# Performance work log

Measured on AMD Instinct MI355X. Metric: run time of the kernel, lower is better.

Reference implementation:

```python
import jax, jax.numpy as jnp
import numpy as np

N, E, CIN, COUT = 100000, 1600000, 64, 128
EPS = 1e-5  # torch BatchNorm default


def setup_inputs() -> dict:
    key = jax.random.key(0)
    ks = jax.random.split(key, 16)
    s = 0.1
    x = jax.random.normal(ks[0], (N, CIN), jnp.float32)
    src = jax.random.randint(ks[1], (E,), 0, N, dtype=jnp.int32)
    dst = jax.random.randint(ks[2], (E,), 0, N, dtype=jnp.int32)
    edge_index = jnp.stack([src, dst])  # [2, E]
    return {
        "x": x,
        "edge_index": edge_index,
        # conv0: GraphConv(CIN -> COUT)
        "W_root0": jax.random.normal(ks[3], (COUT, CIN), jnp.float32) * s,
        "W_nbr0": jax.random.normal(ks[4], (COUT, CIN), jnp.float32) * s,
        "b0": jnp.zeros((COUT,), jnp.float32),
        # bn0
        "g0": jnp.ones((COUT,), jnp.float32),
        "be0": jnp.zeros((COUT,), jnp.float32),
        # conv1: GraphConv(COUT -> COUT)
        "W_root1": jax.random.normal(ks[5], (COUT, COUT), jnp.float32) * s,
        "W_nbr1": jax.random.normal(ks[6], (COUT, COUT), jnp.float32) * s,
        "b1": jnp.zeros((COUT,), jnp.float32),
        # bn1
        "g1": jnp.ones((COUT,), jnp.float32),
        "be1": jnp.zeros((COUT,), jnp.float32),
        # residual 1x1 conv (Conv1d(CIN, COUT, 1))
        "Wlin": jax.random.normal(ks[7], (COUT, CIN), jnp.float32) * s,
        "blin": jnp.zeros((COUT,), jnp.float32),
    }


def graph_conv(x, src, dst, W_root, W_nbr, b):
    # PyG GraphConv: out_i = W_root x_i + W_nbr * sum_{j: (j->i) in E} x_j + b
    agg = jax.ops.segment_sum(x[src], dst, num_segments=N)  # scatter-add over edges
    return x @ W_root.T + agg @ W_nbr.T + b


def batch_norm(x, gamma, beta):
    # training-mode BatchNorm over the node dimension (biased variance)
    mu = jnp.mean(x, axis=0)
    var = jnp.mean(jnp.square(x - mu), axis=0)
    return (x - mu) * jax.lax.rsqrt(var + EPS) * gamma + beta


def reference(x, edge_index, W_root0, W_nbr0, b0, g0, be0,
              W_root1, W_nbr1, b1, g1, be1, Wlin, blin):
    src, dst = edge_index[0], edge_index[1]
    y = batch_norm(graph_conv(x, src, dst, W_root0, W_nbr0, b0), g0, be0)
    y = jax.nn.relu(y)
    y = batch_norm(graph_conv(y, src, dst, W_root1, W_nbr1, b1), g1, be1)
    out = y + (x @ Wlin.T + blin)  # 1x1 Conv1d residual projection
    return jax.nn.relu(out)
```

## Files before the change

kernel.cpp:

```cpp
#include <hip/hip_runtime.h>
#include <stdint.h>


#define CIN 64
#define COUT 128
#define BN_EPS 1e-5f
#define CURPAD 32
#define PCPAD 32
#define SPAD 32
#define PSH 8
#define PNODES (1 << PSH)
#define MAXP 512

typedef unsigned short u16;
typedef short short8 __attribute__((ext_vector_type(8)));
typedef float f32x4 __attribute__((ext_vector_type(4)));

__device__ __forceinline__ float bf2f(u16 u) {
    union { unsigned int i; float f; } v; v.i = ((unsigned int)u) << 16; return v.f;
}
__device__ __forceinline__ u16 f2bf(float f) {
    union { float f; unsigned int i; } v; v.f = f;
    unsigned int r = v.i + 0x7fffu + ((v.i >> 16) & 1u);
    return (u16)(r >> 16);
}
__device__ __forceinline__ float lo16(unsigned int w) { return bf2f((u16)(w & 0xffffu)); }
__device__ __forceinline__ float hi16(unsigned int w) { return bf2f((u16)(w >> 16)); }

template<bool BF> __device__ __forceinline__ float ldf(const void* p, long i) {
    if (BF) return bf2f(((const u16*)p)[i]);
    return ((const float*)p)[i];
}
template<bool BF> __device__ __forceinline__ short8 ld8(const void* p, long i) {
    if (BF) return *(const short8*)((const u16*)p + i);
    const float* f = (const float*)p + i;
    short8 r;
#pragma unroll
    for (int j = 0; j < 8; ++j) r[j] = (short)f2bf(f[j]);
    return r;
}

__device__ __forceinline__ void acc8(float* a, uint4 w) {
    a[0] += lo16(w.x); a[1] += hi16(w.x);
    a[2] += lo16(w.y); a[3] += hi16(w.y);
    a[4] += lo16(w.z); a[5] += hi16(w.z);
    a[6] += lo16(w.w); a[7] += hi16(w.w);
}

__global__ void k_detect(const unsigned int* __restrict__ x, int* __restrict__ flag) {
    int lane = threadIdx.x;
    int cnt = 0;
#pragma unroll
    for (int i = 0; i < 8; ++i) {
        unsigned int w = x[lane * 8 + i];
        unsigned int e0 = (w >> 7) & 0xFFu, e1 = (w >> 23) & 0xFFu;
        cnt += (e0 >= 0x60u && e0 <= 0x8Eu);
        cnt += (e1 >= 0x60u && e1 <= 0x8Eu);
    }
    for (int o = 32; o; o >>= 1) cnt += __shfl_down(cnt, o);
    if (lane == 0) *flag = (cnt > 850) ? 1 : 0;
}

__global__ __launch_bounds__(256) void k_phist(const int* __restrict__ dst,
                                               int* __restrict__ pcount, int E, int np) {
    __shared__ int h[MAXP];
    for (int i = threadIdx.x; i < np; i += 256) h[i] = 0;
    __syncthreads();
    int stride = gridDim.x * 256;
    for (int e = blockIdx.x * 256 + threadIdx.x; e < E; e += stride)
        atomicAdd(&h[dst[e] >> PSH], 1);
    __syncthreads();
    for (int i = threadIdx.x; i < np; i += 256)
        if (h[i]) atomicAdd(&pcount[i * PCPAD], h[i]);
}

__global__ void k_pscan(const int* __restrict__ pcount, int* __restrict__ pstart,
                        int* __restrict__ pcursor, int np, int E) {
    __shared__ int s[MAXP];
    int t = threadIdx.x;
    int v = (t < np) ? pcount[t * PCPAD] : 0;
    s[t] = v; __syncthreads();
    for (int o = 1; o < MAXP; o <<= 1) {
        int u = (t >= o) ? s[t - o] : 0;
        __syncthreads(); s[t] += u; __syncthreads();
    }
    if (t < np) {
        int ex = s[t] - v;
        pstart[t] = ex;
        pcursor[t * CURPAD] = ex;
    }
    if (t == 0) pstart[np] = E;
}

__global__ __launch_bounds__(256) void k_pfill(const int* __restrict__ src,
        const int* __restrict__ dst, int* __restrict__ pcursor,
        unsigned int* __restrict__ barr, int E, int np) {
    __shared__ int cnt[MAXP], gb[MAXP], loc[MAXP];
    int tid = threadIdx.x;
    int base = blockIdx.x * 4096;
    for (int i = tid; i < np; i += 256) { cnt[i] = 0; loc[i] = 0; }
    __syncthreads();
    int pk[16]; unsigned int rec[16];
#pragma unroll
    for (int k = 0; k < 16; ++k) {
        int e = base + k * 256 + tid;
        if (e < E) {
            int d = dst[e];
            pk[k] = d >> PSH;
            rec[k] = ((unsigned int)(d & (PNODES - 1)) << 20) | (unsigned int)src[e];
            atomicAdd(&cnt[pk[k]], 1);
        } else pk[k] = -1;
    }
    __syncthreads();
    for (int i = tid; i < np; i += 256)
        if (cnt[i]) gb[i] = atomicAdd(&pcursor[i * CURPAD], cnt[i]);
    __syncthreads();
#pragma unroll
    for (int k = 0; k < 16; ++k) {
        if (pk[k] >= 0) {
            int off = atomicAdd(&loc[pk[k]], 1);
            barr[gb[pk[k]] + off] = rec[k];
        }
    }
}

__global__ __launch_bounds__(256) void k_psort(const unsigned int* __restrict__ barr,
        const int* __restrict__ pstart, int* __restrict__ csr,
        int* __restrict__ row_start, int n, int np, int E) {
    __shared__ int hist[PNODES], curs[PNODES], tsum[256];
    int tid = threadIdx.x;
    int p = blockIdx.x;
    int e0 = pstart[p], e1 = pstart[p + 1];
    int node0 = p << PSH;
    hist[tid] = 0;
    __syncthreads();
    for (int t = e0 + tid; t < e1; t += 256)
        atomicAdd(&hist[barr[t] >> 20], 1);
    __syncthreads();
    int v = hist[tid];
    tsum[tid] = v; __syncthreads();
    for (int o = 1; o < 256; o <<= 1) {
        int u = (tid >= o) ? tsum[tid - o] : 0;
        __syncthreads(); tsum[tid] += u; __syncthreads();
    }
    int ex = tsum[tid] - v;
    curs[tid] = ex;
    int nd = node0 + tid;
    if (nd < n) row_start[nd] = e0 + ex;
    if (p == np - 1 && tid == 0) row_start[n] = E;
    __syncthreads();
    for (int t = e0 + tid; t < e1; t += 256) {
        unsigned int rec = barr[t];
        int pos = atomicAdd(&curs[rec >> 20], 1);
        csr[e0 + pos] = (int)(rec & 0xFFFFF);
    }
}

template<bool BF>
__device__ __forceinline__ void agg0_impl(const void* x, const int* rs, const int* csr,
                                          u16* agg, int n) {
    int i = blockIdx.x * 4 + (threadIdx.x >> 6);
    if (i >= n) return;
    int lane = threadIdx.x & 63;
    int slot = lane >> 4, cp = lane & 15;
    int b = rs[i], e = rs[i + 1];
    if (BF) {
        const unsigned int* x32 = (const unsigned int*)x;
        float acc[4] = {0.f, 0.f, 0.f, 0.f};
        int t = b + slot;
        for (; t + 12 < e; t += 16) {
            int j0 = csr[t], j1 = csr[t + 4], j2 = csr[t + 8], j3 = csr[t + 12];
            uint2 w0 = *((const uint2*)(x32 + (long)j0 * 32) + cp);
            uint2 w1 = *((const uint2*)(x32 + (long)j1 * 32) + cp);
            uint2 w2 = *((const uint2*)(x32 + (long)j2 * 32) + cp);
            uint2 w3 = *((const uint2*)(x32 + (long)j3 * 32) + cp);
            acc[0] += lo16(w0.x) + lo16(w1.x); acc[1] += hi16(w0.x) + hi16(w1.x);
            acc[2] += lo16(w0.y) + lo16(w1.y); acc[3] += hi16(w0.y) + hi16(w1.y);
            acc[0] += lo16(w2.x) + lo16(w3.x); acc[1] += hi16(w2.x) + hi16(w3.x);
            acc[2] += lo16(w2.y) + lo16(w3.y); acc[3] += hi16(w2.y) + hi16(w3.y);
        }
        for (; t < e; t += 4) {
            int j0 = csr[t];
            uint2 w0 = *((const uint2*)(x32 + (long)j0 * 32) + cp);
            acc[0] += lo16(w0.x); acc[1] += hi16(w0.x);
            acc[2] += lo16(w0.y); acc[3] += hi16(w0.y);
        }
#pragma unroll
        for (int k = 0; k < 4; ++k) {
            acc[k] += __shfl_xor(acc[k], 16);
            acc[k] += __shfl_xor(acc[k], 32);
        }
        if (slot == 0) {
            uint2 o;
            o.x = (unsigned int)f2bf(acc[0]) | ((unsigned int)f2bf(acc[1]) << 16);
            o.y = (unsigned int)f2bf(acc[2]) | ((unsigned int)f2bf(acc[3]) << 16);
            *((uint2*)((unsigned int*)agg + (long)i * 32) + cp) = o;
        }
    } else {
        float acc[4] = {0.f, 0.f, 0.f, 0.f};
        int t = b + slot;
        for (; t + 12 < e; t += 16) {
            int j0 = csr[t], j1 = csr[t + 4], j2 = csr[t + 8], j3 = csr[t + 12];
            float4 w0 = *((const float4*)((const float*)x + (long)j0 * 64) + cp);
            float4 w1 = *((const float4*)((const float*)x + (long)j1 * 64) + cp);
            float4 w2 = *((const float4*)((const float*)x + (long)j2 * 64) + cp);
            float4 w3 = *((const float4*)((const float*)x + (long)j3 * 64) + cp);
            acc[0] += (w0.x + w1.x) + (w2.x + w3.x);
            acc[1] += (w0.y + w1.y) + (w2.y + w3.y);
            acc[2] += (w0.z + w1.z) + (w2.z + w3.z);
            acc[3] += (w0.w + w1.w) + (w2.w + w3.w);
        }
        for (; t < e; t += 4) {
            int j0 = csr[t];
            float4 w0 = *((const float4*)((const float*)x + (long)j0 * 64) + cp);
            acc[0] += w0.x; acc[1] += w0.y; acc[2] += w0.z; acc[3] += w0.w;
        }
#pragma unroll
        for (int k = 0; k < 4; ++k) {
            acc[k] += __shfl_xor(acc[k], 16);
            acc[k] += __shfl_xor(acc[k], 32);
        }
        if (slot == 0) {
            uint2 o;
            o.x = (unsigned int)f2bf(acc[0]) | ((unsigned int)f2bf(acc[1]) << 16);
            o.y = (unsigned int)f2bf(acc[2]) | ((unsigned int)f2bf(acc[3]) << 16);
            *((uint2*)((unsigned int*)agg + (long)i * 32) + cp) = o;
        }
    }
}

__global__ __launch_bounds__(256) void k_agg0(const int* __restrict__ flag,
        const void* x, const int* __restrict__ rs, const int* __restrict__ csr,
        u16* __restrict__ agg, int n) {
    if (*flag) agg0_impl<true >(x, rs, csr, agg, n);
    else       agg0_impl<false>(x, rs, csr, agg, n);
}

__global__ __launch_bounds__(256) void k_y0p(unsigned int* __restrict__ y0,
        const float* __restrict__ sc, const float* __restrict__ sh, long nq) {
    long idx = (long)blockIdx.x * 256 + threadIdx.x;
    int colq = threadIdx.x & 15;
    float s8[8], h8[8];
#pragma unroll
    for (int j = 0; j < 8; ++j) { s8[j] = sc[colq * 8 + j]; h8[j] = sh[colq * 8 + j]; }
    long stride = (long)gridDim.x * 256;
    uint4* p = (uint4*)y0;
    for (; idx < nq; idx += stride) {
        uint4 w = p[idx];
        unsigned int r[4] = {w.x, w.y, w.z, w.w};
        uint4 o;
        unsigned int* po = (unsigned int*)&o;
#pragma unroll
        for (int d = 0; d < 4; ++d) {
            float a = fmaxf(lo16(r[d]) * s8[2 * d]     + h8[2 * d],     0.f);
            float b = fmaxf(hi16(r[d]) * s8[2 * d + 1] + h8[2 * d + 1], 0.f);
            po[d] = (unsigned int)f2bf(a) | ((unsigned int)f2bf(b) << 16);
        }
        p[idx] = o;
    }
}

__global__ __launch_bounds__(256) void k_agg1(const u16* __restrict__ y0p,
        const int* __restrict__ rs, const int* __restrict__ csr,
        u16* __restrict__ agg, int n) {
    int i0 = blockIdx.x * 8 + ((threadIdx.x >> 6) << 1);
    if (i0 >= n) return;
    int lane = threadIdx.x & 63;
    int slot = lane >> 4, cp = lane & 15;
    const unsigned int* y32 = (const unsigned int*)y0p;
    int i1 = i0 + 1;
    int bA = rs[i0], eA = rs[i0 + 1];
    int bB = eA, eB = (i1 < n) ? rs[i1 + 1] : eA;

    float aA[8] = {0.f, 0.f, 0.f, 0.f, 0.f, 0.f, 0.f, 0.f};
    float aB[8] = {0.f, 0.f, 0.f, 0.f, 0.f, 0.f, 0.f, 0.f};
    int tA = bA + slot, tB = bB + slot;

    while (tA + 12 < eA && tB + 12 < eB) {
        int ja0 = csr[tA], ja1 = csr[tA + 4], ja2 = csr[tA + 8], ja3 = csr[tA + 12];
        int jb0 = csr[tB], jb1 = csr[tB + 4], jb2 = csr[tB + 8], jb3 = csr[tB + 12];
        uint4 wa0 = *((const uint4*)(y32 + (long)ja0 * 64) + cp);
        uint4 wa1 = *((const uint4*)(y32 + (long)ja1 * 64) + cp);
        uint4 wa2 = *((const uint4*)(y32 + (long)ja2 * 64) + cp);
        uint4 wa3 = *((const uint4*)(y32 + (long)ja3 * 64) + cp);
        uint4 wb0 = *((const uint4*)(y32 + (long)jb0 * 64) + cp);
        uint4 wb1 = *((const uint4*)(y32 + (long)jb1 * 64) + cp);
        uint4 wb2 = *((const uint4*)(y32 + (long)jb2 * 64) + cp);
        uint4 wb3 = *((const uint4*)(y32 + (long)jb3 * 64) + cp);
        acc8(aA, wa0); acc8(aA, wa1); acc8(aA, wa2); acc8(aA, wa3);
        acc8(aB, wb0); acc8(aB, wb1); acc8(aB, wb2); acc8(aB, wb3);
        tA += 16; tB += 16;
    }
    for (; tA + 12 < eA; tA += 16) {
        int j0 = csr[tA], j1 = csr[tA + 4], j2 = csr[tA + 8], j3 = csr[tA + 12];
        uint4 w0 = *((const uint4*)(y32 + (long)j0 * 64) + cp);
        uint4 w1 = *((const uint4*)(y32 + (long)j1 * 64) + cp);
        uint4 w2 = *((const uint4*)(y32 + (long)j2 * 64) + cp);
        uint4 w3 = *((const uint4*)(y32 + (long)j3 * 64) + cp);
        acc8(aA, w0); acc8(aA, w1); acc8(aA, w2); acc8(aA, w3);
    }
    for (; tA < eA; tA += 4) {
        uint4 w0 = *((const uint4*)(y32 + (long)csr[tA] * 64) + cp);
        acc8(aA, w0);
    }
    for (; tB + 12 < eB; tB += 16) {
        int j0 = csr[tB], j1 = csr[tB + 4], j2 = csr[tB + 8], j3 = csr[tB + 12];
        uint4 w0 = *((const uint4*)(y32 + (long)j0 * 64) + cp);
        uint4 w1 = *((const uint4*)(y32 + (long)j1 * 64) + cp);
        uint4 w2 = *((const uint4*)(y32 + (long)j2 * 64) + cp);
        uint4 w3 = *((const uint4*)(y32 + (long)j3 * 64) + cp);
        acc8(aB, w0); acc8(aB, w1); acc8(aB, w2); acc8(aB, w3);
    }
    for (; tB < eB; tB += 4) {
        uint4 w0 = *((const uint4*)(y32 + (long)csr[tB] * 64) + cp);
        acc8(aB, w0);
    }
#pragma unroll
    for (int k = 0; k < 8; ++k) {
        aA[k] += __shfl_xor(aA[k], 16);
        aA[k] += __shfl_xor(aA[k], 32);
        aB[k] += __shfl_xor(aB[k], 16);
        aB[k] += __shfl_xor(aB[k], 32);
    }
    if (slot == 0) {
        uint4 o;
        o.x = (unsigned int)f2bf(aA[0]) | ((unsigned int)f2bf(aA[1]) << 16);
        o.y = (unsigned int)f2bf(aA[2]) | ((unsigned int)f2bf(aA[3]) << 16);
        o.z = (unsigned int)f2bf(aA[4]) | ((unsigned int)f2bf(aA[5]) << 16);
        o.w = (unsigned int)f2bf(aA[6]) | ((unsigned int)f2bf(aA[7]) << 16);
        *((uint4*)((unsigned int*)agg + (long)i0 * 64) + cp) = o;
        if (i1 < n) {
            uint4 p;
            p.x = (unsigned int)f2bf(aB[0]) | ((unsigned int)f2bf(aB[1]) << 16);
            p.y = (unsigned int)f2bf(aB[2]) | ((unsigned int)f2bf(aB[3]) << 16);
            p.z = (unsigned int)f2bf(aB[4]) | ((unsigned int)f2bf(aB[5]) << 16);
            p.w = (unsigned int)f2bf(aB[6]) | ((unsigned int)f2bf(aB[7]) << 16);
            *((uint4*)((unsigned int*)agg + (long)i1 * 64) + cp) = p;
        }
    }
}

template<bool BF>
__device__ __forceinline__ void gemm0_impl(const void* x, const u16* agg,
                                           const void* Wr, const void* Wn,
                                           u16* y0, float* sumP, float* sqP,
                                           int n, int nch, u16* lds) {
    const int ST = 130;
    int tid = threadIdx.x;
    int wave = tid >> 6, lane = tid & 63, lr = lane & 15, q = lane >> 4;

    short8 wf[2][4];
#pragma unroll
    for (int i = 0; i < 2; ++i) {
        int c = (2 * wave + i) * 16 + lr;
#pragma unroll
        for (int ks = 0; ks < 4; ++ks) {
            const void* W = (ks < 2) ? Wr : Wn;
            wf[i][ks] = ld8<BF>(W, (long)c * CIN + (ks & 1) * 32 + q * 8);
        }
    }

    const int rowb = tid >> 3, wb = tid & 7;
    const int rowf = tid >> 4, wfc = tid & 15;
    short8 rbx[2]; float4 rfx[4]; short8 rag[2];

    auto regload = [&](long chunk0) {
        if (BF) {
#pragma unroll
            for (int i = 0; i < 2; ++i) {
                long rg = chunk0 + rowb + i * 32; if (rg > n - 1) rg = n - 1;
                rbx[i] = *(const short8*)((const u16*)x + rg * CIN + wb * 8);
            }
        } else {
#pragma unroll
            for (int i = 0; i < 4; ++i) {
                long rg = chunk0 + rowf + i * 16; if (rg > n - 1) rg = n - 1;
                rfx[i] = *(const float4*)((const float*)x + rg * CIN + wfc * 4);
            }
        }
#pragma unroll
        for (int i = 0; i < 2; ++i) {
            long rg = chunk0 + rowb + i * 32; if (rg > n - 1) rg = n - 1;
            rag[i] = *(const short8*)(agg + rg * CIN + wb * 8);
        }
    };

    float st[2] = {0.f, 0.f}, sq[2] = {0.f, 0.f};
    int ch = blockIdx.x;
    if (ch < nch) regload((long)ch * 64);
    for (; ch < nch; ch += gridDim.x) {
        long chunk0 = (long)ch * 64;
        __syncthreads();
        if (BF) {
#pragma unroll
            for (int i = 0; i < 2; ++i)
                *(short8*)(lds + (rowb + i * 32) * ST + wb * 8) = rbx[i];
        } else {
#pragma unroll
            for (int i = 0; i < 4; ++i) {
                u16* d = lds + (rowf + i * 16) * ST + wfc * 4;
                d[0] = f2bf(rfx[i].x); d[1] = f2bf(rfx[i].y);
                d[2] = f2bf(rfx[i].z); d[3] = f2bf(rfx[i].w);
            }
        }
#pragma unroll
        for (int i = 0; i < 2; ++i)
            *(short8*)(lds + (rowb + i * 32) * ST + 64 + wb * 8) = rag[i];
        __syncthreads();
        long nxt = (long)ch + gridDim.x;
        if (nxt < nch) regload(nxt * 64);

#pragma unroll
        for (int t = 0; t < 4; ++t) {
            short8 a[4];
#pragma unroll
            for (int ks = 0; ks < 4; ++ks)
                a[ks] = *(const short8*)(lds + (t * 16 + lr) * ST + ks * 32 + q * 8);
#pragma unroll
            for (int i = 0; i < 2; ++i) {
                f32x4 acc = {0.f, 0.f, 0.f, 0.f};
#pragma unroll
                for (int ks = 0; ks < 4; ++ks)
                    acc = __builtin_amdgcn_mfma_f32_16x16x32_bf16(a[ks], wf[i][ks], acc, 0, 0, 0);
                int c = (2 * wave + i) * 16 + lr;
#pragma unroll
                for (int r = 0; r < 4; ++r) {
                    long row = chunk0 + t * 16 + q * 4 + r;
                    if (row < n) {
                        y0[row * COUT + c] = f2bf(acc[r]);
                        st[i] += acc[r]; sq[i] += acc[r] * acc[r];
                    }
                }
            }
        }
    }
#pragma unroll
    for (int i = 0; i < 2; ++i) {
        st[i] += __shfl_xor(st[i], 16); st[i] += __shfl_xor(st[i], 32);
        sq[i] += __shfl_xor(sq[i], 16); sq[i] += __shfl_xor(sq[i], 32);
    }
    if (q == 0) {
#pragma unroll
        for (int i = 0; i < 2; ++i) {
            int c = (2 * wave + i) * 16 + lr;
            atomicAdd(&sumP[c * SPAD], st[i]);
            atomicAdd(&sqP[c * SPAD], sq[i]);
        }
    }
}

__global__ __launch_bounds__(256) void k_gemm0(const int* __restrict__ flag,
        const void* x, const u16* __restrict__ agg, const void* Wr, const void* Wn,
        u16* __restrict__ y0, float* __restrict__ sumP, float* __restrict__ sqP,
        int n, int nch) {
    __shared__ u16 lds[64 * 130];
    if (*flag) gemm0_impl<true >(x, agg, Wr, Wn, y0, sumP, sqP, n, nch, lds);
    else       gemm0_impl<false>(x, agg, Wr, Wn, y0, sumP, sqP, n, nch, lds);
}

template<bool BF>
__device__ __forceinline__ void gemm1_impl(const u16* y0p, const u16* agg,
                                           const void* Wr, const void* Wn,
                                           u16* y1, float* sumP, float* sqP,
                                           int n, int nch) {
    int tid = threadIdx.x;
    int wave = tid >> 6, lane = tid & 63, lr = lane & 15, q = lane >> 4;

    short8 wf[2][8];
#pragma unroll
    for (int i = 0; i < 2; ++i) {
        int c = (2 * wave + i) * 16 + lr;
#pragma unroll
        for (int ks = 0; ks < 8; ++ks) {
            const void* W = (ks < 4) ? Wr : Wn;
            wf[i][ks] = ld8<BF>(W, (long)c * COUT + (ks & 3) * 32 + q * 8);
        }
    }

    float st[2] = {0.f, 0.f}, sq[2] = {0.f, 0.f};
    for (int ch = blockIdx.x; ch < nch; ch += gridDim.x) {
        long chunk0 = (long)ch * 64;
#pragma unroll
        for (int t = 0; t < 4; ++t) {
            long rg = chunk0 + t * 16 + lr; if (rg > n - 1) rg = n - 1;
            short8 a[8];
#pragma unroll
            for (int ks = 0; ks < 4; ++ks)
                a[ks] = *(const short8*)(y0p + rg * COUT + ks * 32 + q * 8);
#pragma unroll
            for (int ks = 0; ks < 4; ++ks)
                a[4 + ks] = *(const short8*)(agg + rg * COUT + ks * 32 + q * 8);
#pragma unroll
            for (int i = 0; i < 2; ++i) {
                f32x4 acc = {0.f, 0.f, 0.f, 0.f};
#pragma unroll
                for (int ks = 0; ks < 8; ++ks)
                    acc = __builtin_amdgcn_mfma_f32_16x16x32_bf16(a[ks], wf[i][ks], acc, 0, 0, 0);
                int c = (2 * wave + i) * 16 + lr;
#pragma unroll
                for (int r = 0; r < 4; ++r) {
                    long row = chunk0 + t * 16 + q * 4 + r;
                    if (row < n) {
                        y1[row * COUT + c] = f2bf(acc[r]);
                        st[i] += acc[r]; sq[i] += acc[r] * acc[r];
                    }
                }
            }
        }
    }
#pragma unroll
    for (int i = 0; i < 2; ++i) {
        st[i] += __shfl_xor(st[i], 16); st[i] += __shfl_xor(st[i], 32);
        sq[i] += __shfl_xor(sq[i], 16); sq[i] += __shfl_xor(sq[i], 32);
    }
    if (q == 0) {
#pragma unroll
        for (int i = 0; i < 2; ++i) {
            int c = (2 * wave + i) * 16 + lr;
            atomicAdd(&sumP[c * SPAD], st[i]);
            atomicAdd(&sqP[c * SPAD], sq[i]);
        }
    }
}

__global__ __launch_bounds__(256) void k_gemm1(const int* __restrict__ flag,
        const u16* __restrict__ y0p, const u16* __restrict__ agg,
        const void* Wr, const void* Wn,
        u16* y1_bf , u16* y1_ws,
        float* __restrict__ sumP, float* __restrict__ sqP, int n, int nch) {
    u16* y1 = *flag ? y1_bf : y1_ws;
    if (*flag) gemm1_impl<true >(y0p, agg, Wr, Wn, y1, sumP, sqP, n, nch);
    else       gemm1_impl<false>(y0p, agg, Wr, Wn, y1, sumP, sqP, n, nch);
}

__global__ void k_bnfin(const int* __restrict__ flag,
                        const float* __restrict__ sumP, const float* __restrict__ sqP,
                        const void* g, const void* be,
                        float* __restrict__ scale, float* __restrict__ shift, int n) {
    int c = threadIdx.x;
    bool bf = (*flag != 0);
    float inv = 1.f / (float)n;
    float mu = sumP[c * SPAD] * inv;
    float var = fmaxf(sqP[c * SPAD] * inv - mu * mu, 0.f);
    float gv = bf ? bf2f(((const u16*)g)[c]) : ((const float*)g)[c];
    float bv = bf ? bf2f(((const u16*)be)[c]) : ((const float*)be)[c];
    float sc = gv * rsqrtf(var + BN_EPS);
    scale[c] = sc;
    shift[c] = bv - mu * sc;
}

template<bool BF>
__device__ __forceinline__ void final_impl(const void* x, const u16* y1,
                                           const void* Wlin, const void* blin,
                                           const float* sc, const float* sh,
                                           void* out, int n, int nch, u16* lds) {
    const int ST = 194;
    int tid = threadIdx.x;
    int wave = tid >> 6, lane = tid & 63, lr = lane & 15, q = lane >> 4;

    short8 wf[2][2];
    float blc[2], scc[2], shc[2];
#pragma unroll
    for (int i = 0; i < 2; ++i) {
        int c = (2 * wave + i) * 16 + lr;
#pragma unroll
        for (int ks = 0; ks < 2; ++ks)
            wf[i][ks] = ld8<BF>(Wlin, (long)c * CIN + ks * 32 + q * 8);
        blc[i] = ldf<BF>(blin, c);
        scc[i] = sc[c]; shc[i] = sh[c];
    }

    const int rowb = tid >> 3, wb = tid & 7;
    const int rowf = tid >> 4, wfc = tid & 15;
    const int rowy = tid >> 4, wy = tid & 15;
    short8 rbx[2]; float4 rfx[4]; short8 ry[4];

    auto regload = [&](long chunk0) {
        if (BF) {
#pragma unroll
            for (int i = 0; i < 2; ++i) {
                long rg = chunk0 + rowb + i * 32; if (rg > n - 1) rg = n - 1;
                rbx[i] = *(const short8*)((const u16*)x + rg * CIN + wb * 8);
            }
        } else {
#pragma unroll
            for (int i = 0; i < 4; ++i) {
                long rg = chunk0 + rowf + i * 16; if (rg > n - 1) rg = n - 1;
                rfx[i] = *(const float4*)((const float*)x + rg * CIN + wfc * 4);
            }
        }
#pragma unroll
        for (int i = 0; i < 4; ++i) {
            long rg = chunk0 + rowy + i * 16; if (rg > n - 1) rg = n - 1;
            ry[i] = *(const short8*)(y1 + rg * COUT + wy * 8);
        }
    };

    int ch = blockIdx.x;
    if (ch < nch) regload((long)ch * 64);
    for (; ch < nch; ch += gridDim.x) {
        long chunk0 = (long)ch * 64;
        __syncthreads();
        if (BF) {
#pragma unroll
            for (int i = 0; i < 2; ++i)
                *(short8*)(lds + (rowb + i * 32) * ST + wb * 8) = rbx[i];
        } else {
#pragma unroll
            for (int i = 0; i < 4; ++i) {
                u16* d = lds + (rowf + i * 16) * ST + wfc * 4;
                d[0] = f2bf(rfx[i].x); d[1] = f2bf(rfx[i].y);
                d[2] = f2bf(rfx[i].z); d[3] = f2bf(rfx[i].w);
            }
        }
#pragma unroll
        for (int i = 0; i < 4; ++i)
            *(short8*)(lds + (rowy + i * 16) * ST + 64 + wy * 8) = ry[i];
        __syncthreads();
        long nxt = (long)ch + gridDim.x;
        if (nxt < nch) regload(nxt * 64);

#pragma unroll
        for (int t = 0; t < 4; ++t) {
            short8 a[2];
#pragma unroll
            for (int ks = 0; ks < 2; ++ks)
                a[ks] = *(const short8*)(lds + (t * 16 + lr) * ST + ks * 32 + q * 8);
#pragma unroll
            for (int i = 0; i < 2; ++i) {
                f32x4 acc = {0.f, 0.f, 0.f, 0.f};
                acc = __builtin_amdgcn_mfma_f32_16x16x32_bf16(a[0], wf[i][0], acc, 0, 0, 0);
                acc = __builtin_amdgcn_mfma_f32_16x16x32_bf16(a[1], wf[i][1], acc, 0, 0, 0);
                int c = (2 * wave + i) * 16 + lr;
#pragma unroll
                for (int r = 0; r < 4; ++r) {
                    long row = chunk0 + t * 16 + q * 4 + r;
                    if (row < n) {
                        float yv = bf2f(lds[(t * 16 + q * 4 + r) * ST + 64 + c]);
                        float v = acc[r] + blc[i] + yv * scc[i] + shc[i];
                        v = fmaxf(v, 0.f);
                        if (BF) ((u16*)out)[row * COUT + c] = f2bf(v);
                        else    ((float*)out)[row * COUT + c] = v;
                    }
                }
            }
        }
    }
}

__global__ __launch_bounds__(256) void k_final(const int* __restrict__ flag,
        const void* x, const void* Wlin, const void* blin,
        const u16* y1_bf , const u16* y1_ws,
        const float* __restrict__ sc, const float* __restrict__ sh,
        void* out, int n, int nch) {
    __shared__ u16 lds[64 * 194];
    const u16* y1 = *flag ? y1_bf : y1_ws;
    if (*flag) final_impl<true >(x, y1, Wlin, blin, sc, sh, out, n, nch, lds);
    else       final_impl<false>(x, y1, Wlin, blin, sc, sh, out, n, nch, lds);
}

extern "C" void kernel_launch(void* const* d_in, const int* in_sizes, int n_in,
                              void* d_out, int out_size, void* d_ws, size_t ws_size,
                              hipStream_t stream) {
    (void)n_in; (void)out_size; (void)ws_size;
    const void* x    = d_in[0];
    const int*  ei   = (const int*)d_in[1];
    const void* Wr0  = d_in[2];
    const void* Wn0  = d_in[3];
    const void* g0   = d_in[5];
    const void* be0  = d_in[6];
    const void* Wr1  = d_in[7];
    const void* Wn1  = d_in[8];
    const void* g1   = d_in[10];
    const void* be1  = d_in[11];
    const void* Wlin = d_in[12];
    const void* blin = d_in[13];

    const int N = in_sizes[0] / CIN;
    const int E = in_sizes[1] / 2;
    const int* src = ei;
    const int* dst = ei + E;
    const int NP = (N + PNODES - 1) >> PSH;

    char* base = (char*)d_ws;
    size_t off = 0;
    auto carve = [&](size_t bytes) -> void* {
        void* p = base + off;
        off = (off + bytes + 255) & ~(size_t)255;
        return p;
    };
    int*   flag      = (int*)carve(256);
    int*   pcount    = (int*)carve(MAXP * PCPAD * sizeof(int));
    int*   pstart    = (int*)carve((MAXP + 1) * sizeof(int));
    int*   pcursor   = (int*)carve(MAXP * CURPAD * sizeof(int));
    float* statsP    = (float*)carve(4 * 128 * SPAD * sizeof(float));
    float* scsh      = (float*)carve(512 * sizeof(float));
    int*   row_start = (int*)carve((size_t)(N + 1) * sizeof(int));
    unsigned int* barr = (unsigned int*)carve((size_t)E * sizeof(int));
    int*   csr       = (int*)carve((size_t)E * sizeof(int));
    u16*   aggu      = (u16*)carve((size_t)N * COUT * sizeof(u16));
    u16*   y0        = (u16*)carve((size_t)N * COUT * sizeof(u16));
    u16*   y1_ws     = (u16*)carve((size_t)N * COUT * sizeof(u16));

    float* sum0P = statsP;
    float* sq0P  = statsP + 128 * SPAD;
    float* sum1P = statsP + 256 * SPAD;
    float* sq1P  = statsP + 384 * SPAD;

    hipMemsetAsync(pcount, 0, MAXP * PCPAD * sizeof(int), stream);
    hipMemsetAsync(statsP, 0, 4 * 128 * SPAD * sizeof(float), stream);

    const int nwb = (N + 3) / 4;
    const int nwb2 = (N + 7) / 8;
    const int nch = (N + 63) / 64;
    const int ntl = (E + 4095) / 4096;
    const int G   = nch < 1024 ? nch : 1024;
    const long nq = (long)N * 16;
    int g2 = (int)((nq + 255) / 256); if (g2 > 2048) g2 = 2048;

    k_detect<<<1, 64, 0, stream>>>((const unsigned int*)x, flag);

    k_phist<<<256, 256, 0, stream>>>(dst, pcount, E, NP);
    k_pscan<<<1, MAXP, 0, stream>>>(pcount, pstart, pcursor, NP, E);
    k_pfill<<<ntl, 256, 0, stream>>>(src, dst, pcursor, barr, E, NP);
    k_psort<<<NP, 256, 0, stream>>>(barr, pstart, csr, row_start, N, NP, E);

    k_agg0 <<<nwb, 256, 0, stream>>>(flag, x, row_start, csr, aggu, N);
    k_gemm0<<<G, 256, 0, stream>>>(flag, x, aggu, Wr0, Wn0, y0,
                                   sum0P, sq0P, N, nch);
    k_bnfin<<<1, 128, 0, stream>>>(flag, sum0P, sq0P, g0, be0,
                                   scsh, scsh + 128, N);

    k_y0p<<<g2, 256, 0, stream>>>((unsigned int*)y0, scsh, scsh + 128, nq);

    k_agg1 <<<nwb2, 256, 0, stream>>>(y0, row_start, csr, aggu, N);
    k_gemm1<<<G, 256, 0, stream>>>(flag, y0, aggu, Wr1, Wn1,
                                   (u16*)d_out, y1_ws, sum1P, sq1P, N, nch);
    k_bnfin<<<1, 128, 0, stream>>>(flag, sum1P, sq1P, g1, be1,
                                   scsh + 256, scsh + 384, N);

    k_final<<<G, 256, 0, stream>>>(flag, x, Wlin, blin,
                                   (const u16*)d_out, y1_ws,
                                   scsh + 256, scsh + 384, d_out, N, nch);
}
```

Baseline: 402.6 us.

## Pre-convert x to bf16 once and read it directly in aggregation and GEMMs

Adds a kernel that converts x to a bf16 copy up front, so agg0, gemm0 and final all read a compact bf16 array. This removes the per-kernel fp32/bf16 branches and the LDS staging of x. gemm0 now loads its A fragments straight from global memory with no LDS or register prefetch, and agg1 goes back to one node per wave. The cost is an extra pass over x, and the gemm0 loads may be less coalesced with less latency hiding.

New measurement: 393.1 us. 1.02x faster.

```diff
diff --git a/kernel.cpp b/kernel.cpp
--- a/kernel.cpp
+++ b/kernel.cpp
@@ -61,6 +61,28 @@
     if (lane == 0) *flag = (cnt > 850) ? 1 : 0;
 }
 
+__global__ __launch_bounds__(256) void k_xbf(const int* __restrict__ flag,
+        const void* __restrict__ x, u16* __restrict__ xb, long n8) {
+    long idx = (long)blockIdx.x * 256 + threadIdx.x;
+    long stride = (long)gridDim.x * 256;
+    uint4* dst = (uint4*)xb;
+    if (*flag) {
+        const uint4* src = (const uint4*)x;
+        for (; idx < n8; idx += stride) dst[idx] = src[idx];
+    } else {
+        const float4* src = (const float4*)x;
+        for (; idx < n8; idx += stride) {
+            float4 a = src[idx * 2], b = src[idx * 2 + 1];
+            uint4 o;
+            o.x = (unsigned int)f2bf(a.x) | ((unsigned int)f2bf(a.y) << 16);
+            o.y = (unsigned int)f2bf(a.z) | ((unsigned int)f2bf(a.w) << 16);
+            o.z = (unsigned int)f2bf(b.x) | ((unsigned int)f2bf(b.y) << 16);
+            o.w = (unsigned int)f2bf(b.z) | ((unsigned int)f2bf(b.w) << 16);
+            dst[idx] = o;
+        }
+    }
+}
+
 __global__ __launch_bounds__(256) void k_phist(const int* __restrict__ dst,
                                                int* __restrict__ pcount, int E, int np) {
     __shared__ int h[MAXP];
@@ -156,84 +178,45 @@
     }
 }
 
-template<bool BF>
-__device__ __forceinline__ void agg0_impl(const void* x, const int* rs, const int* csr,
-                                          u16* agg, int n) {
+__global__ __launch_bounds__(256) void k_agg0(const u16* __restrict__ xb,
+        const int* __restrict__ rs, const int* __restrict__ csr,
+        u16* __restrict__ agg, int n) {
     int i = blockIdx.x * 4 + (threadIdx.x >> 6);
     if (i >= n) return;
     int lane = threadIdx.x & 63;
     int slot = lane >> 4, cp = lane & 15;
+    const unsigned int* x32 = (const unsigned int*)xb;
     int b = rs[i], e = rs[i + 1];
-    if (BF) {
-        const unsigned int* x32 = (const unsigned int*)x;
-        float acc[4] = {0.f, 0.f, 0.f, 0.f};
-        int t = b + slot;
-        for (; t + 12 < e; t += 16) {
-            int j0 = csr[t], j1 = csr[t + 4], j2 = csr[t + 8], j3 = csr[t + 12];
-            uint2 w0 = *((const uint2*)(x32 + (long)j0 * 32) + cp);
-            uint2 w1 = *((const uint2*)(x32 + (long)j1 * 32) + cp);
-            uint2 w2 = *((const uint2*)(x32 + (long)j2 * 32) + cp);
-            uint2 w3 = *((const uint2*)(x32 + (long)j3 * 32) + cp);
-            acc[0] += lo16(w0.x) + lo16(w1.x); acc[1] += hi16(w0.x) + hi16(w1.x);
-            acc[2] += lo16(w0.y) + lo16(w1.y); acc[3] += hi16(w0.y) + hi16(w1.y);
-            acc[0] += lo16(w2.x) + lo16(w3.x); acc[1] += hi16(w2.x) + hi16(w3.x);
-            acc[2] += lo16(w2.y) + lo16(w3.y); acc[3] += hi16(w2.y) + hi16(w3.y);
-        }
-        for (; t < e; t += 4) {
-            int j0 = csr[t];
-            uint2 w0 = *((const uint2*)(x32 + (long)j0 * 32) + cp);
-            acc[0] += lo16(w0.x); acc[1] += hi16(w0.x);
-            acc[2] += lo16(w0.y); acc[3] += hi16(w0.y);
-        }
-#pragma unroll
-        for (int k = 0; k < 4; ++k) {
-            acc[k] += __shfl_xor(acc[k], 16);
-            acc[k] += __shfl_xor(acc[k], 32);
-        }
-        if (slot == 0) {
-            uint2 o;
-            o.x = (unsigned int)f2bf(acc[0]) | ((unsigned int)f2bf(acc[1]) << 16);
-            o.y = (unsigned int)f2bf(acc[2]) | ((unsigned int)f2bf(acc[3]) << 16);
-            *((uint2*)((unsigned int*)agg + (long)i * 32) + cp) = o;
-        }
-    } else {
-        float acc[4] = {0.f, 0.f, 0.f, 0.f};
-        int t = b + slot;
-        for (; t + 12 < e; t += 16) {
-            int j0 = csr[t], j1 = csr[t + 4], j2 = csr[t + 8], j3 = csr[t + 12];
-            float4 w0 = *((const float4*)((const float*)x + (long)j0 * 64) + cp);
-            float4 w1 = *((const float4*)((const float*)x + (long)j1 * 64) + cp);
-            float4 w2 = *((const float4*)((const float*)x + (long)j2 * 64) + cp);
-            float4 w3 = *((const float4*)((const float*)x + (long)j3 * 64) + cp);
-            acc[0] += (w0.x + w1.x) + (w2.x + w3.x);
-            acc[1] += (w0.y + w1.y) + (w2.y + w3.y);
-            acc[2] += (w0.z + w1.z) + (w2.z + w3.z);
-            acc[3] += (w0.w + w1.w) + (w2.w + w3.w);
-        }
-        for (; t < e; t += 4) {
-            int j0 = csr[t];
-            float4 w0 = *((const float4*)((const float*)x + (long)j0 * 64) + cp);
-            acc[0] += w0.x; acc[1] += w0.y; acc[2] += w0.z; acc[3] += w0.w;
-        }
-#pragma unroll
-        for (int k = 0; k < 4; ++k) {
-            acc[k] += __shfl_xor(acc[k], 16);
-            acc[k] += __shfl_xor(acc[k], 32);
-        }
-        if (slot == 0) {
-            uint2 o;
-            o.x = (unsigned int)f2bf(acc[0]) | ((unsigned int)f2bf(acc[1]) << 16);
-            o.y = (unsigned int)f2bf(acc[2]) | ((unsigned int)f2bf(acc[3]) << 16);
-            *((uint2*)((unsigned int*)agg + (long)i * 32) + cp) = o;
-        }
-    }
-}
-
-__global__ __launch_bounds__(256) void k_agg0(const int* __restrict__ flag,
-        const void* x, const int* __restrict__ rs, const int* __restrict__ csr,
-        u16* __restrict__ agg, int n) {
-    if (*flag) agg0_impl<true >(x, rs, csr, agg, n);
-    else       agg0_impl<false>(x, rs, csr, agg, n);
+    float acc[4] = {0.f, 0.f, 0.f, 0.f};
+    int t = b + slot;
+    for (; t + 12 < e; t += 16) {
+        int j0 = csr[t], j1 = csr[t + 4], j2 = csr[t + 8], j3 = csr[t + 12];
+        uint2 w0 = *((const uint2*)(x32 + (long)j0 * 32) + cp);
+        uint2 w1 = *((const uint2*)(x32 + (long)j1 * 32) + cp);
+        uint2 w2 = *((const uint2*)(x32 + (long)j2 * 32) + cp);
+        uint2 w3 = *((const uint2*)(x32 + (long)j3 * 32) + cp);
+        acc[0] += lo16(w0.x) + lo16(w1.x); acc[1] += hi16(w0.x) + hi16(w1.x);
+        acc[2] += lo16(w0.y) + lo16(w1.y); acc[3] += hi16(w0.y) + hi16(w1.y);
+        acc[0] += lo16(w2.x) + lo16(w3.x); acc[1] += hi16(w2.x) + hi16(w3.x);
+        acc[2] += lo16(w2.y) + lo16(w3.y); acc[3] += hi16(w2.y) + hi16(w3.y);
+    }
+    for (; t < e; t += 4) {
+        int j0 = csr[t];
+        uint2 w0 = *((const uint2*)(x32 + (long)j0 * 32) + cp);
+        acc[0] += lo16(w0.x); acc[1] += hi16(w0.x);
+        acc[2] += lo16(w0.y); acc[3] += hi16(w0.y);
+    }
+#pragma unroll
+    for (int k = 0; k < 4; ++k) {
+        acc[k] += __shfl_xor(acc[k], 16);
+        acc[k] += __shfl_xor(acc[k], 32);
+    }
+    if (slot == 0) {
+        uint2 o;
+        o.x = (unsigned int)f2bf(acc[0]) | ((unsigned int)f2bf(acc[1]) << 16);
+        o.y = (unsigned int)f2bf(acc[2]) | ((unsigned int)f2bf(acc[3]) << 16);
+        *((uint2*)((unsigned int*)agg + (long)i * 32) + cp) = o;
+    }
 }
 
 __global__ __launch_bounds__(256) void k_y0p(unsigned int* __restrict__ y0,
@@ -263,89 +246,47 @@
 __global__ __launch_bounds__(256) void k_agg1(const u16* __restrict__ y0p,
         const int* __restrict__ rs, const int* __restrict__ csr,
         u16* __restrict__ agg, int n) {
-    int i0 = blockIdx.x * 8 + ((threadIdx.x >> 6) << 1);
-    if (i0 >= n) return;
+    int i = blockIdx.x * 4 + (threadIdx.x >> 6);
+    if (i >= n) return;
     int lane = threadIdx.x & 63;
     int slot = lane >> 4, cp = lane & 15;
     const unsigned int* y32 = (const unsigned int*)y0p;
-    int i1 = i0 + 1;
-    int bA = rs[i0], eA = rs[i0 + 1];
-    int bB = eA, eB = (i1 < n) ? rs[i1 + 1] : eA;
-
-    float aA[8] = {0.f, 0.f, 0.f, 0.f, 0.f, 0.f, 0.f, 0.f};
-    float aB[8] = {0.f, 0.f, 0.f, 0.f, 0.f, 0.f, 0.f, 0.f};
-    int tA = bA + slot, tB = bB + slot;
-
-    while (tA + 12 < eA && tB + 12 < eB) {
-        int ja0 = csr[tA], ja1 = csr[tA + 4], ja2 = csr[tA + 8], ja3 = csr[tA + 12];
-        int jb0 = csr[tB], jb1 = csr[tB + 4], jb2 = csr[tB + 8], jb3 = csr[tB + 12];
-        uint4 wa0 = *((const uint4*)(y32 + (long)ja0 * 64) + cp);
-        uint4 wa1 = *((const uint4*)(y32 + (long)ja1 * 64) + cp);
-        uint4 wa2 = *((const uint4*)(y32 + (long)ja2 * 64) + cp);
-        uint4 wa3 = *((const uint4*)(y32 + (long)ja3 * 64) + cp);
-        uint4 wb0 = *((const uint4*)(y32 + (long)jb0 * 64) + cp);
-        uint4 wb1 = *((const uint4*)(y32 + (long)jb1 * 64) + cp);
-        uint4 wb2 = *((const uint4*)(y32 + (long)jb2 * 64) + cp);
-        uint4 wb3 = *((const uint4*)(y32 + (long)jb3 * 64) + cp);
-        acc8(aA, wa0); acc8(aA, wa1); acc8(aA, wa2); acc8(aA, wa3);
-        acc8(aB, wb0); acc8(aB, wb1); acc8(aB, wb2); acc8(aB, wb3);
-        tA += 16; tB += 16;
-    }
-    for (; tA + 12 < eA; tA += 16) {
-        int j0 = csr[tA], j1 = csr[tA + 4], j2 = csr[tA + 8], j3 = csr[tA + 12];
+    int b = rs[i], e = rs[i + 1];
+    float acc[8] = {0.f, 0.f, 0.f, 0.f, 0.f, 0.f, 0.f, 0.f};
+    int t = b + slot;
+    for (; t + 12 < e; t += 16) {
+        int j0 = csr[t], j1 = csr[t + 4], j2 = csr[t + 8], j3 = csr[t + 12];
         uint4 w0 = *((const uint4*)(y32 + (long)j0 * 64) + cp);
         uint4 w1 = *((const uint4*)(y32 + (long)j1 * 64) + cp);
         uint4 w2 = *((const uint4*)(y32 + (long)j2 * 64) + cp);
         uint4 w3 = *((const uint4*)(y32 + (long)j3 * 64) + cp);
-        acc8(aA, w0); acc8(aA, w1); acc8(aA, w2); acc8(aA, w3);
-    }
-    for (; tA < eA; tA += 4) {
-        uint4 w0 = *((const uint4*)(y32 + (long)csr[tA] * 64) + cp);
-        acc8(aA, w0);
-    }
-    for (; tB + 12 < eB; tB += 16) {
-        int j0 = csr[tB], j1 = csr[tB + 4], j2 = csr[tB + 8], j3 = csr[tB + 12];
+        acc8(acc, w0); acc8(acc, w1); acc8(acc, w2); acc8(acc, w3);
+    }
+    for (; t < e; t += 4) {
+        int j0 = csr[t];
         uint4 w0 = *((const uint4*)(y32 + (long)j0 * 64) + cp);
-        uint4 w1 = *((const uint4*)(y32 + (long)j1 * 64) + cp);
-        uint4 w2 = *((const uint4*)(y32 + (long)j2 * 64) + cp);
-        uint4 w3 = *((const uint4*)(y32 + (long)j3 * 64) + cp);
-        acc8(aB, w0); acc8(aB, w1); acc8(aB, w2); acc8(aB, w3);
-    }
-    for (; tB < eB; tB += 4) {
-        uint4 w0 = *((const uint4*)(y32 + (long)csr[tB] * 64) + cp);
-        acc8(aB, w0);
+        acc8(acc, w0);
     }
 #pragma unroll
     for (int k = 0; k < 8; ++k) {
-        aA[k] += __shfl_xor(aA[k], 16);
-        aA[k] += __shfl_xor(aA[k], 32);
-        aB[k] += __shfl_xor(aB[k], 16);
-        aB[k] += __shfl_xor(aB[k], 32);
+        acc[k] += __shfl_xor(acc[k], 16);
+        acc[k] += __shfl_xor(acc[k], 32);
     }
     if (slot == 0) {
         uint4 o;
-        o.x = (unsigned int)f2bf(aA[0]) | ((unsigned int)f2bf(aA[1]) << 16);
-        o.y = (unsigned int)f2bf(aA[2]) | ((unsigned int)f2bf(aA[3]) << 16);
-        o.z = (unsigned int)f2bf(aA[4]) | ((unsigned int)f2bf(aA[5]) << 16);
-        o.w = (unsigned int)f2bf(aA[6]) | ((unsigned int)f2bf(aA[7]) << 16);
-        *((uint4*)((unsigned int*)agg + (long)i0 * 64) + cp) = o;
-        if (i1 < n) {
-            uint4 p;
-            p.x = (unsigned int)f2bf(aB[0]) | ((unsigned int)f2bf(aB[1]) << 16);
-            p.y = (unsigned int)f2bf(aB[2]) | ((unsigned int)f2bf(aB[3]) << 16);
-            p.z = (unsigned int)f2bf(aB[4]) | ((unsigned int)f2bf(aB[5]) << 16);
-            p.w = (unsigned int)f2bf(aB[6]) | ((unsigned int)f2bf(aB[7]) << 16);
-            *((uint4*)((unsigned int*)agg + (long)i1 * 64) + cp) = p;
-        }
+        o.x = (unsigned int)f2bf(acc[0]) | ((unsigned int)f2bf(acc[1]) << 16);
+        o.y = (unsigned int)f2bf(acc[2]) | ((unsigned int)f2bf(acc[3]) << 16);
+        o.z = (unsigned int)f2bf(acc[4]) | ((unsigned int)f2bf(acc[5]) << 16);
+        o.w = (unsigned int)f2bf(acc[6]) | ((unsigned int)f2bf(acc[7]) << 16);
+        *((uint4*)((unsigned int*)agg + (long)i * 64) + cp) = o;
     }
 }
 
 template<bool BF>
-__device__ __forceinline__ void gemm0_impl(const void* x, const u16* agg,
+__device__ __forceinline__ void gemm0_impl(const u16* xb, const u16* agg,
                                            const void* Wr, const void* Wn,
                                            u16* y0, float* sumP, float* sqP,
-                                           int n, int nch, u16* lds) {
-    const int ST = 130;
+                                           int n, int nch) {
     int tid = threadIdx.x;
     int wave = tid >> 6, lane = tid & 63, lr = lane & 15, q = lane >> 4;
 
@@ -360,62 +301,19 @@
         }
     }
 
-    const int rowb = tid >> 3, wb = tid & 7;
-    const int rowf = tid >> 4, wfc = tid & 15;
-    short8 rbx[2]; float4 rfx[4]; short8 rag[2];
-
-    auto regload = [&](long chunk0) {
-        if (BF) {
-#pragma unroll
-            for (int i = 0; i < 2; ++i) {
-                long rg = chunk0 + rowb + i * 32; if (rg > n - 1) rg = n - 1;
-                rbx[i] = *(const short8*)((const u16*)x + rg * CIN + wb * 8);
-            }
-        } else {
-#pragma unroll
-            for (int i = 0; i < 4; ++i) {
-                long rg = chunk0 + rowf + i * 16; if (rg > n - 1) rg = n - 1;
-                rfx[i] = *(const float4*)((const float*)x + rg * CIN + wfc * 4);
-            }
-        }
-#pragma unroll
-        for (int i = 0; i < 2; ++i) {
-            long rg = chunk0 + rowb + i * 32; if (rg > n - 1) rg = n - 1;
-            rag[i] = *(const short8*)(agg + rg * CIN + wb * 8);
-        }
-    };
-
     float st[2] = {0.f, 0.f}, sq[2] = {0.f, 0.f};
-    int ch = blockIdx.x;
-    if (ch < nch) regload((long)ch * 64);
-    for (; ch < nch; ch += gridDim.x) {
+    for (int ch = blockIdx.x; ch < nch; ch += gridDim.x) {
         long chunk0 = (long)ch * 64;
-        __syncthreads();
-        if (BF) {
-#pragma unroll
-            for (int i = 0; i < 2; ++i)
-                *(short8*)(lds + (rowb + i * 32) * ST + wb * 8) = rbx[i];
-        } else {
-#pragma unroll
-            for (int i = 0; i < 4; ++i) {
-                u16* d = lds + (rowf + i * 16) * ST + wfc * 4;
-                d[0] = f2bf(rfx[i].x); d[1] = f2bf(rfx[i].y);
-                d[2] = f2bf(rfx[i].z); d[3] = f2bf(rfx[i].w);
-            }
-        }
-#pragma unroll
-        for (int i = 0; i < 2; ++i)
-            *(short8*)(lds + (rowb + i * 32) * ST + 64 + wb * 8) = rag[i];
-        __syncthreads();
-        long nxt = (long)ch + gridDim.x;
-        if (nxt < nch) regload(nxt * 64);
-
 #pragma unroll
         for (int t = 0; t < 4; ++t) {
+            long rg = chunk0 + t * 16 + lr; if (rg > n - 1) rg = n - 1;
             short8 a[4];
 #pragma unroll
-            for (int ks = 0; ks < 4; ++ks)
-                a[ks] = *(const short8*)(lds + (t * 16 + lr) * ST + ks * 32 + q * 8);
+            for (int ks = 0; ks < 2; ++ks)
+                a[ks] = *(const short8*)(xb + rg * CIN + ks * 32 + q * 8);
+#pragma unroll
+            for (int ks = 0; ks < 2; ++ks)
+                a[2 + ks] = *(const short8*)(agg + rg * CIN + ks * 32 + q * 8);
 #pragma unroll
             for (int i = 0; i < 2; ++i) {
                 f32x4 acc = {0.f, 0.f, 0.f, 0.f};
@@ -450,12 +348,12 @@
 }
 
 __global__ __launch_bounds__(256) void k_gemm0(const int* __restrict__ flag,
-        const void* x, const u16* __restrict__ agg, const void* Wr, const void* Wn,
+        const u16* __restrict__ xb, const u16* __restrict__ agg,
+        const void* Wr, const void* Wn,
         u16* __restrict__ y0, float* __restrict__ sumP, float* __restrict__ sqP,
         int n, int nch) {
-    __shared__ u16 lds[64 * 130];
-    if (*flag) gemm0_impl<true >(x, agg, Wr, Wn, y0, sumP, sqP, n, nch, lds);
-    else       gemm0_impl<false>(x, agg, Wr, Wn, y0, sumP, sqP, n, nch, lds);
+    if (*flag) gemm0_impl<true >(xb, agg, Wr, Wn, y0, sumP, sqP, n, nch);
+    else       gemm0_impl<false>(xb, agg, Wr, Wn, y0, sumP, sqP, n, nch);
 }
 
 template<bool BF>
@@ -550,11 +448,11 @@
 }
 
 template<bool BF>
-__device__ __forceinline__ void final_impl(const void* x, const u16* y1,
+__device__ __forceinline__ void final_impl(const u16* xb, const u16* y1,
                                            const void* Wlin, const void* blin,
                                            const float* sc, const float* sh,
                                            void* out, int n, int nch, u16* lds) {
-    const int ST = 194;
+    const int ST = 130;
     int tid = threadIdx.x;
     int wave = tid >> 6, lane = tid & 63, lr = lane & 15, q = lane >> 4;
 
@@ -570,25 +468,10 @@
         scc[i] = sc[c]; shc[i] = sh[c];
     }
 
-    const int rowb = tid >> 3, wb = tid & 7;
-    const int rowf = tid >> 4, wfc = tid & 15;
     const int rowy = tid >> 4, wy = tid & 15;
-    short8 rbx[2]; float4 rfx[4]; short8 ry[4];
+    short8 ry[4];
 
     auto regload = [&](long chunk0) {
-        if (BF) {
-#pragma unroll
-            for (int i = 0; i < 2; ++i) {
-                long rg = chunk0 + rowb + i * 32; if (rg > n - 1) rg = n - 1;
-                rbx[i] = *(const short8*)((const u16*)x + rg * CIN + wb * 8);
-            }
-        } else {
-#pragma unroll
-            for (int i = 0; i < 4; ++i) {
-                long rg = chunk0 + rowf + i * 16; if (rg > n - 1) rg = n - 1;
-                rfx[i] = *(const float4*)((const float*)x + rg * CIN + wfc * 4);
-            }
-        }
 #pragma unroll
         for (int i = 0; i < 4; ++i) {
             long rg = chunk0 + rowy + i * 16; if (rg > n - 1) rg = n - 1;
@@ -601,31 +484,20 @@
     for (; ch < nch; ch += gridDim.x) {
         long chunk0 = (long)ch * 64;
         __syncthreads();
-        if (BF) {
-#pragma unroll
-            for (int i = 0; i < 2; ++i)
-                *(short8*)(lds + (rowb + i * 32) * ST + wb * 8) = rbx[i];
-        } else {
-#pragma unroll
-            for (int i = 0; i < 4; ++i) {
-                u16* d = lds + (rowf + i * 16) * ST + wfc * 4;
-                d[0] = f2bf(rfx[i].x); d[1] = f2bf(rfx[i].y);
-                d[2] = f2bf(rfx[i].z); d[3] = f2bf(rfx[i].w);
-            }
-        }
 #pragma unroll
         for (int i = 0; i < 4; ++i)
-            *(short8*)(lds + (rowy + i * 16) * ST + 64 + wy * 8) = ry[i];
+            *(short8*)(lds + (rowy + i * 16) * ST + wy * 8) = ry[i];
         __syncthreads();
         long nxt = (long)ch + gridDim.x;
         if (nxt < nch) regload(nxt * 64);
 
 #pragma unroll
         for (int t = 0; t < 4; ++t) {
+            long rg = chunk0 + t * 16 + lr; if (rg > n - 1) rg = n - 1;
             short8 a[2];
 #pragma unroll
             for (int ks = 0; ks < 2; ++ks)
-                a[ks] = *(const short8*)(lds + (t * 16 + lr) * ST + ks * 32 + q * 8);
+                a[ks] = *(const short8*)(xb + rg * CIN + ks * 32 + q * 8);
 #pragma unroll
             for (int i = 0; i < 2; ++i) {
                 f32x4 acc = {0.f, 0.f, 0.f, 0.f};
@@ -636,7 +508,7 @@
                 for (int r = 0; r < 4; ++r) {
                     long row = chunk0 + t * 16 + q * 4 + r;
                     if (row < n) {
-                        float yv = bf2f(lds[(t * 16 + q * 4 + r) * ST + 64 + c]);
+                        float yv = bf2f(lds[(t * 16 + q * 4 + r) * ST + c]);
                         float v = acc[r] + blc[i] + yv * scc[i] + shc[i];
                         v = fmaxf(v, 0.f);
                         if (BF) ((u16*)out)[row * COUT + c] = f2bf(v);
@@ -649,14 +521,14 @@
 }
 
 __global__ __launch_bounds__(256) void k_final(const int* __restrict__ flag,
-        const void* x, const void* Wlin, const void* blin,
+        const u16* __restrict__ xb, const void* Wlin, const void* blin,
         const u16* y1_bf , const u16* y1_ws,
         const float* __restrict__ sc, const float* __restrict__ sh,
         void* out, int n, int nch) {
-    __shared__ u16 lds[64 * 194];
+    __shared__ u16 lds[64 * 130];
     const u16* y1 = *flag ? y1_bf : y1_ws;
-    if (*flag) final_impl<true >(x, y1, Wlin, blin, sc, sh, out, n, nch, lds);
-    else       final_impl<false>(x, y1, Wlin, blin, sc, sh, out, n, nch, lds);
+    if (*flag) final_impl<true >(xb, y1, Wlin, blin, sc, sh, out, n, nch, lds);
+    else       final_impl<false>(xb, y1, Wlin, blin, sc, sh, out, n, nch, lds);
 }
 
 extern "C" void kernel_launch(void* const* d_in, const int* in_sizes, int n_in,
@@ -698,6 +570,7 @@
     int*   row_start = (int*)carve((size_t)(N + 1) * sizeof(int));
     unsigned int* barr = (unsigned int*)carve((size_t)E * sizeof(int));
     int*   csr       = (int*)carve((size_t)E * sizeof(int));
+    u16*   xb        = (u16*)carve((size_t)N * CIN * sizeof(u16));
     u16*   aggu      = (u16*)carve((size_t)N * COUT * sizeof(u16));
     u16*   y0        = (u16*)carve((size_t)N * COUT * sizeof(u16));
     u16*   y1_ws     = (u16*)carve((size_t)N * COUT * sizeof(u16));
@@ -711,35 +584,37 @@
     hipMemsetAsync(statsP, 0, 4 * 128 * SPAD * sizeof(float), stream);
 
     const int nwb = (N + 3) / 4;
-    const int nwb2 = (N + 7) / 8;
     const int nch = (N + 63) / 64;
     const int ntl = (E + 4095) / 4096;
     const int G   = nch < 1024 ? nch : 1024;
     const long nq = (long)N * 16;
+    const long n8 = (long)N * CIN / 8;
     int g2 = (int)((nq + 255) / 256); if (g2 > 2048) g2 = 2048;
+    int g3 = (int)((n8 + 255) / 256); if (g3 > 2048) g3 = 2048;
 
     k_detect<<<1, 64, 0, stream>>>((const unsigned int*)x, flag);
+    k_xbf<<<g3, 256, 0, stream>>>(flag, x, xb, n8);
 
     k_phist<<<256, 256, 0, stream>>>(dst, pcount, E, NP);
     k_pscan<<<1, MAXP, 0, stream>>>(pcount, pstart, pcursor, NP, E);
     k_pfill<<<ntl, 256, 0, stream>>>(src, dst, pcursor, barr, E, NP);
     k_psort<<<NP, 256, 0, stream>>>(barr, pstart, csr, row_start, N, NP, E);
 
-    k_agg0 <<<nwb, 256, 0, stream>>>(flag, x, row_start, csr, aggu, N);
-    k_gemm0<<<G, 256, 0, stream>>>(flag, x, aggu, Wr0, Wn0, y0,
+    k_agg0 <<<nwb, 256, 0, stream>>>(xb, row_start, csr, aggu, N);
+    k_gemm0<<<G, 256, 0, stream>>>(flag, xb, aggu, Wr0, Wn0, y0,
                                    sum0P, sq0P, N, nch);
     k_bnfin<<<1, 128, 0, stream>>>(flag, sum0P, sq0P, g0, be0,
                                    scsh, scsh + 128, N);
 
     k_y0p<<<g2, 256, 0, stream>>>((unsigned int*)y0, scsh, scsh + 128, nq);
 
-    k_agg1 <<<nwb2, 256, 0, stream>>>(y0, row_start, csr, aggu, N);
+    k_agg1 <<<nwb, 256, 0, stream>>>(y0, row_start, csr, aggu, N);
     k_gemm1<<<G, 256, 0, stream>>>(flag, y0, aggu, Wr1, Wn1,
                                    (u16*)d_out, y1_ws, sum1P, sq1P, N, nch);
     k_bnfin<<<1, 128, 0, stream>>>(flag, sum1P, sq1P, g1, be1,
                                    scsh + 256, scsh + 384, N);
 
-    k_final<<<G, 256, 0, stream>>>(flag, x, Wlin, blin,
+    k_final<<<G, 256, 0, stream>>>(flag, xb, Wlin, blin,
                                    (const u16*)d_out, y1_ws,
                                    scsh + 256, scsh + 384, d_out, N, nch);
 }
```
